# Kernel optimization log

Measured on AMD Instinct MI355X. Metric: run time of the kernel, lower is better.

The kernel has to match this reference:

```python
import jax, jax.numpy as jnp
import numpy as np

N_LEVELS = 16
N_FEATURES = 2
MIN_RES = 16
MAX_RES = 512
HASH_SIZE = 19
TABLE_SIZE = 2 ** HASH_SIZE
# per-level grid resolutions (geometric progression, matches torch buffer)
RESOLUTIONS = [int(MIN_RES * (MAX_RES / MIN_RES) ** (i / (N_LEVELS - 1))) for i in range(N_LEVELS)]
# 8 cube-corner offsets, [8, 3] (same ordering as torch.meshgrid indexing='ij')
OFFSETS = np.stack(np.meshgrid(np.array([0, 1]), np.array([0, 1]), np.array([0, 1]), indexing='ij')).reshape(3, -1).T.astype(np.int64)
PRIMES = np.array([1, 2654435761, 805459861], dtype=np.int64)


def setup_inputs() -> dict:
    key = jax.random.key(0)
    k1, k2 = jax.random.split(key)
    N = 1 << 20  # ~1M sample points (e.g., 4096 rays x 256 samples)
    x = jax.random.uniform(k1, (N, 3), dtype=jnp.float32, minval=-1.0, maxval=1.0)
    tables = jax.random.uniform(k2, (N_LEVELS, TABLE_SIZE, N_FEATURES), dtype=jnp.float32, minval=-1e-4, maxval=1e-4)
    return {"x": x, "tables": tables}


def reference(x, tables):
    x = jnp.clip(x.astype(jnp.float32), -1.0, 1.0)  # [N, 3]
    offsets = jnp.asarray(OFFSETS)                  # [8, 3] int64
    primes = jnp.asarray(PRIMES)                    # [3] int64
    outs = []
    for i, res in enumerate(RESOLUTIONS):
        coords = x * res                            # [N, 3]
        cf = jnp.floor(coords)
        lc = coords - cf                            # fractional part, [N, 3]
        # 8 corner integer coords, wrapped into [0, res): [N, 8, 3]
        corners = (cf.astype(jnp.int64)[:, None, :] + offsets[None]) % res
        corners_f = corners.astype(jnp.float32) / res
        # spatial hash: quantize to [0, 2^18) grid then prime-multiply hash
        q = ((corners_f + 1.0) * 0.5 * (2.0 ** 18)).astype(jnp.int64)
        hashed = (q * primes).sum(-1) % TABLE_SIZE  # [N, 8]
        feats = tables[i][hashed]                   # gather, [N, 8, F]
        # trilinear weights: prod over dims of (1-lc) if offset==0 else lc
        w = jnp.where(offsets[None] == 0, 1.0 - lc[:, None, :], lc[:, None, :]).prod(-1)  # [N, 8]
        outs.append((w[..., None] * feats).sum(1))  # [N, F]
    return jnp.concatenate(outs, axis=-1)           # [N, L*F]
```

## Files before the change

### kernel.cpp

```cpp
#include <hip/hip_runtime.h>


static constexpr int      kNLevels   = 16;
static constexpr unsigned kTableSize = 1u << 19;
static constexpr unsigned kMask      = kTableSize - 1u;
static constexpr unsigned kP1        = 2654435761u;
static constexpr unsigned kP2        = 805459861u;

static constexpr int kNBins = 32768;

typedef float v4f __attribute__((ext_vector_type(4)));
typedef float v2f __attribute__((ext_vector_type(2)));

constexpr int RES_[kNLevels]  = {16, 20, 25, 32, 40, 50, 64, 80,
                                 101, 127, 161, 203, 256, 322, 406, 512};
constexpr int QOFF_[kNLevels] = {0, 16, 36, 61, 93, 133, 183, 247,
                                 327, 428, 555, 716, 919, 1175, 1497, 1903};
static constexpr int kQTot = 2415;

constexpr unsigned qval_rcp(int c, int res) {
    const float r = 1.0f / (float)res;
    const float v = (float)c * r;
    const float s = ((v + 1.0f) * 0.5f) * 262144.0f;
    return (unsigned)s;
}

struct QTab {
    unsigned v[kQTot];
    constexpr QTab() : v{} {
        int o = 0;
        for (int i = 0; i < kNLevels; ++i) {
            for (int c = 0; c < RES_[i]; ++c) v[o + c] = qval_rcp(c, RES_[i]);
            o += RES_[i];
        }
    }
};
__constant__ QTab QT = QTab();

__device__ __forceinline__ void level_idx_w(
    const int i, const unsigned* __restrict__ sq,
    const float px, const float py, const float pz,
    unsigned* __restrict__ idx, float* __restrict__ w)
{
    const int   res  = RES_[i];
    const float resf = (float)res;
    const unsigned* qt = sq + QOFF_[i];

    const float cxf = px * resf, cyf = py * resf, czf = pz * resf;
    const float fx = floorf(cxf), fy = floorf(cyf), fz = floorf(czf);
    const float lx = cxf - fx, ly = cyf - fy, lz = czf - fz;

    const int ix = (int)fx, iy = (int)fy, iz = (int)fz;
    const int cx0 = ix < 0 ? ix + res : (ix >= res ? ix - res : ix);
    const int cy0 = iy < 0 ? iy + res : (iy >= res ? iy - res : iy);
    const int cz0 = iz < 0 ? iz + res : (iz >= res ? iz - res : iz);
    const int cx1 = (cx0 + 1 == res) ? 0 : cx0 + 1;
    const int cy1 = (cy0 + 1 == res) ? 0 : cy0 + 1;
    const int cz1 = (cz0 + 1 == res) ? 0 : cz0 + 1;

    const unsigned qx0 = qt[cx0], qx1 = qt[cx1];
    const unsigned qy0 = qt[cy0], qy1 = qt[cy1];
    const unsigned qz0 = qt[cz0], qz1 = qt[cz1];

    const unsigned hy0 = qy0 * kP1, hy1 = qy1 * kP1;
    const unsigned hz0 = qz0 * kP2, hz1 = qz1 * kP2;

    const float wx0 = 1.0f - lx, wx1 = lx;
    const float wy0 = 1.0f - ly, wy1 = ly;
    const float wz0 = 1.0f - lz, wz1 = lz;

#pragma unroll
    for (int m = 0; m < 8; ++m) {
        const unsigned h = ((m & 4) ? qx1 : qx0) +
                           ((m & 2) ? hy1 : hy0) +
                           ((m & 1) ? hz1 : hz0);
        idx[m] = h & kMask;
        w[m] = (((m & 4) ? wx1 : wx0) * ((m & 2) ? wy1 : wy0)) *
               ((m & 1) ? wz1 : wz0);
    }
}

__device__ __forceinline__ void encode_point(
    const unsigned* __restrict__ sq, const float* __restrict__ tables,
    float* __restrict__ out, const int n)
{
    float px = out ? 0.0f : 0.0f;
    (void)px;
}

__device__ __forceinline__ unsigned spread5(unsigned x) {
    x &= 0x3ffu;
    x = (x | (x << 16)) & 0x30000FFu;
    x = (x | (x << 8))  & 0x300F00Fu;
    x = (x | (x << 4))  & 0x30C30C3u;
    x = (x | (x << 2))  & 0x9249249u;
    return x;
}

__device__ __forceinline__ unsigned point_bin(const float* __restrict__ x, int n) {
    float px = fminf(fmaxf(x[3 * n + 0], -1.0f), 1.0f);
    float py = fminf(fmaxf(x[3 * n + 1], -1.0f), 1.0f);
    float pz = fminf(fmaxf(x[3 * n + 2], -1.0f), 1.0f);
    int cx = (int)((px + 1.0f) * 16.0f); cx = cx > 31 ? 31 : cx;
    int cy = (int)((py + 1.0f) * 16.0f); cy = cy > 31 ? 31 : cy;
    int cz = (int)((pz + 1.0f) * 16.0f); cz = cz > 31 ? 31 : cz;
    return spread5((unsigned)cx) | (spread5((unsigned)cy) << 1) |
           (spread5((unsigned)cz) << 2);
}

__global__ void zero_kernel(unsigned* __restrict__ p, int n) {
    int i = blockIdx.x * 256 + threadIdx.x;
    if (i < n) p[i] = 0u;
}

__global__ void hist_kernel(const float* __restrict__ x,
                            unsigned* __restrict__ counts, int N) {
    int n = blockIdx.x * 256 + threadIdx.x;
    if (n >= N) return;
    atomicAdd(&counts[point_bin(x, n)], 1u);
}

__global__ __launch_bounds__(1024) void scan_kernel(
    const unsigned* __restrict__ counts, unsigned* __restrict__ cursor) {
    __shared__ unsigned sh[1024];
    const int t = threadIdx.x;
    unsigned loc[32];
    unsigned s = 0;
#pragma unroll
    for (int j = 0; j < 32; ++j) { loc[j] = s; s += counts[t * 32 + j]; }
    sh[t] = s;
    __syncthreads();
    for (int off = 1; off < 1024; off <<= 1) {
        unsigned v = (t >= off) ? sh[t - off] : 0u;
        __syncthreads();
        sh[t] += v;
        __syncthreads();
    }
    const unsigned base = sh[t] - s;
#pragma unroll
    for (int j = 0; j < 32; ++j) cursor[t * 32 + j] = base + loc[j];
}

__global__ void scatter_kernel(const float* __restrict__ x,
                               unsigned* __restrict__ cursor,
                               unsigned* __restrict__ perm, int N) {
    int n = blockIdx.x * 256 + threadIdx.x;
    if (n >= N) return;
    unsigned pos = atomicAdd(&cursor[point_bin(x, n)], 1u);
    perm[pos] = (unsigned)n;
}

template <bool SORTED>
__global__ __launch_bounds__(256, 6) void hashenc_kernel_t(
    const float* __restrict__ x,
    const float* __restrict__ tables,
    float* __restrict__ out,
    const unsigned* __restrict__ perm,
    int N)
{
    __shared__ unsigned sq[kQTot];
    for (int t = threadIdx.x; t < kQTot; t += 256) sq[t] = QT.v[t];
    __syncthreads();

    int bid = blockIdx.x;
    if (SORTED) {
        const int nblk = gridDim.x;
        if ((nblk & 7) == 0) bid = (bid & 7) * (nblk >> 3) + (bid >> 3);
    }
    const int g = bid * 256 + threadIdx.x;
    if (g >= N) return;
    const int n = SORTED ? (int)perm[g] : g;

    float px = x[3 * n + 0];
    float py = x[3 * n + 1];
    float pz = x[3 * n + 2];
    px = fminf(fmaxf(px, -1.0f), 1.0f);
    py = fminf(fmaxf(py, -1.0f), 1.0f);
    pz = fminf(fmaxf(pz, -1.0f), 1.0f);

    v4f* op = (v4f*)(out + (size_t)n * (2 * kNLevels));

#pragma unroll
    for (int ip = 0; ip < kNLevels / 2; ++ip) {
        const int iA = 2 * ip, iB = 2 * ip + 1;

        unsigned ia[8], ib[8];
        float    wa[8], wb[8];
        level_idx_w(iA, sq, px, py, pz, ia, wa);
        level_idx_w(iB, sq, px, py, pz, ib, wb);

        const v2f* tA = (const v2f*)tables + (size_t)iA * kTableSize;
        const v2f* tB = (const v2f*)tables + (size_t)iB * kTableSize;

        v2f fa[8], fb[8];
#pragma unroll
        for (int m = 0; m < 8; ++m) fa[m] = tA[ia[m]];
#pragma unroll
        for (int m = 0; m < 8; ++m) fb[m] = tB[ib[m]];

        float a0 = 0.0f, a1 = 0.0f, b0 = 0.0f, b1 = 0.0f;
#pragma unroll
        for (int m = 0; m < 8; ++m) {
            a0 += wa[m] * fa[m].x;
            a1 += wa[m] * fa[m].y;
        }
#pragma unroll
        for (int m = 0; m < 8; ++m) {
            b0 += wb[m] * fb[m].x;
            b1 += wb[m] * fb[m].y;
        }

        v4f v = {a0, a1, b0, b1};
        op[ip] = v;
    }
}

extern "C" void kernel_launch(void* const* d_in, const int* in_sizes, int n_in,
                              void* d_out, int out_size, void* d_ws, size_t ws_size,
                              hipStream_t stream) {
    const float* x      = (const float*)d_in[0];
    const float* tables = (const float*)d_in[1];
    float*       out    = (float*)d_out;
    const int N = in_sizes[0] / 3;
    const int pb = (N + 255) / 256;

    const size_t need = ((size_t)2 * kNBins + (size_t)N) * sizeof(unsigned);
    if (d_ws != nullptr && ws_size >= need) {
        unsigned* counts = (unsigned*)d_ws;
        unsigned* cursor = counts + kNBins;
        unsigned* perm   = cursor + kNBins;

        hipLaunchKernelGGL(zero_kernel, dim3((kNBins + 255) / 256), dim3(256),
                           0, stream, counts, kNBins);
        hipLaunchKernelGGL(hist_kernel, dim3(pb), dim3(256), 0, stream,
                           x, counts, N);
        hipLaunchKernelGGL(scan_kernel, dim3(1), dim3(1024), 0, stream,
                           counts, cursor);
        hipLaunchKernelGGL(scatter_kernel, dim3(pb), dim3(256), 0, stream,
                           x, cursor, perm, N);
        hipLaunchKernelGGL((hashenc_kernel_t<true>), dim3(pb), dim3(256),
                           0, stream, x, tables, out, perm, N);
    } else {
        hipLaunchKernelGGL((hashenc_kernel_t<false>), dim3(pb), dim3(256),
                           0, stream, x, tables, out, nullptr, N);
    }
}
```

Measured before the change: 991.1 us.

## Split hash encoding into per-level-pair blocks over sorted points

The encoding kernel now launches eight times as many blocks. Each block handles one pair of levels (a small level paired with a large one, g and 15-g) for 256 spatially sorted points. Adjacent blocks work on the same level pair, so each block's gathers stay inside two tables, which should improve cache locality and balance the load. The cost is that every point's coordinates and permutation entry are read eight times, outputs are written as scattered 8-byte stores instead of full rows, and resolution is now a runtime value, so constant folding is lost.

```diff
diff --git a/kernel.cpp b/kernel.cpp
--- a/kernel.cpp
+++ b/kernel.cpp
@@ -37,14 +37,17 @@
 };
 __constant__ QTab QT = QTab();
 
-__device__ __forceinline__ void level_idx_w(
-    const int i, const unsigned* __restrict__ sq,
+__constant__ int cRES[kNLevels]  = {16, 20, 25, 32, 40, 50, 64, 80,
+                                    101, 127, 161, 203, 256, 322, 406, 512};
+__constant__ int cQOFF[kNLevels] = {0, 16, 36, 61, 93, 133, 183, 247,
+                                    327, 428, 555, 716, 919, 1175, 1497, 1903};
+
+__device__ __forceinline__ void level_idx_w_rt(
+    const int res, const unsigned* __restrict__ qt,
     const float px, const float py, const float pz,
     unsigned* __restrict__ idx, float* __restrict__ w)
 {
-    const int   res  = RES_[i];
     const float resf = (float)res;
-    const unsigned* qt = sq + QOFF_[i];
 
     const float cxf = px * resf, cyf = py * resf, czf = pz * resf;
     const float fx = floorf(cxf), fy = floorf(cyf), fz = floorf(czf);
@@ -78,14 +81,6 @@
         w[m] = (((m & 4) ? wx1 : wx0) * ((m & 2) ? wy1 : wy0)) *
                ((m & 1) ? wz1 : wz0);
     }
-}
-
-__device__ __forceinline__ void encode_point(
-    const unsigned* __restrict__ sq, const float* __restrict__ tables,
-    float* __restrict__ out, const int n)
-{
-    float px = out ? 0.0f : 0.0f;
-    (void)px;
 }
 
 __device__ __forceinline__ unsigned spread5(unsigned x) {
@@ -150,26 +145,28 @@
     perm[pos] = (unsigned)n;
 }
 
-template <bool SORTED>
-__global__ __launch_bounds__(256, 6) void hashenc_kernel_t(
+__global__ __launch_bounds__(256, 8) void hashenc_pair_kernel(
     const float* __restrict__ x,
     const float* __restrict__ tables,
     float* __restrict__ out,
     const unsigned* __restrict__ perm,
     int N)
 {
-    __shared__ unsigned sq[kQTot];
-    for (int t = threadIdx.x; t < kQTot; t += 256) sq[t] = QT.v[t];
+    const int g    = blockIdx.x & 7;
+    const int pbid = blockIdx.x >> 3;
+    const int iA = g, iB = 15 - g;
+    const int resA = cRES[iA], resB = cRES[iB];
+    const int qoA  = cQOFF[iA], qoB = cQOFF[iB];
+
+    __shared__ unsigned sq[528];
+    const int tot = resA + resB;
+    for (int t = threadIdx.x; t < tot; t += 256)
+        sq[t] = (t < resA) ? QT.v[qoA + t] : QT.v[qoB + (t - resA)];
     __syncthreads();
 
-    int bid = blockIdx.x;
-    if (SORTED) {
-        const int nblk = gridDim.x;
-        if ((nblk & 7) == 0) bid = (bid & 7) * (nblk >> 3) + (bid >> 3);
-    }
-    const int g = bid * 256 + threadIdx.x;
-    if (g >= N) return;
-    const int n = SORTED ? (int)perm[g] : g;
+    const int gp = pbid * 256 + threadIdx.x;
+    if (gp >= N) return;
+    const int n = (int)perm[gp];
 
     float px = x[3 * n + 0];
     float py = x[3 * n + 1];
@@ -178,6 +175,57 @@
     py = fminf(fmaxf(py, -1.0f), 1.0f);
     pz = fminf(fmaxf(pz, -1.0f), 1.0f);
 
+    unsigned ia[8], ib[8];
+    float    wa[8], wb[8];
+    level_idx_w_rt(resA, sq,        px, py, pz, ia, wa);
+    level_idx_w_rt(resB, sq + resA, px, py, pz, ib, wb);
+
+    const v2f* tA = (const v2f*)tables + (size_t)iA * kTableSize;
+    const v2f* tB = (const v2f*)tables + (size_t)iB * kTableSize;
+
+    v2f fa[8], fb[8];
+#pragma unroll
+    for (int m = 0; m < 8; ++m) fa[m] = tA[ia[m]];
+#pragma unroll
+    for (int m = 0; m < 8; ++m) fb[m] = tB[ib[m]];
+
+    float a0 = 0.0f, a1 = 0.0f, b0 = 0.0f, b1 = 0.0f;
+#pragma unroll
+    for (int m = 0; m < 8; ++m) {
+        a0 += wa[m] * fa[m].x;
+        a1 += wa[m] * fa[m].y;
+    }
+#pragma unroll
+    for (int m = 0; m < 8; ++m) {
+        b0 += wb[m] * fb[m].x;
+        b1 += wb[m] * fb[m].y;
+    }
+
+    v2f* orow = (v2f*)(out + (size_t)n * (2 * kNLevels));
+    v2f va = {a0, a1}; orow[iA] = va;
+    v2f vb = {b0, b1}; orow[iB] = vb;
+}
+
+__global__ __launch_bounds__(256, 6) void hashenc_full_kernel(
+    const float* __restrict__ x,
+    const float* __restrict__ tables,
+    float* __restrict__ out,
+    int N)
+{
+    __shared__ unsigned sq[kQTot];
+    for (int t = threadIdx.x; t < kQTot; t += 256) sq[t] = QT.v[t];
+    __syncthreads();
+
+    const int n = blockIdx.x * 256 + threadIdx.x;
+    if (n >= N) return;
+
+    float px = x[3 * n + 0];
+    float py = x[3 * n + 1];
+    float pz = x[3 * n + 2];
+    px = fminf(fmaxf(px, -1.0f), 1.0f);
+    py = fminf(fmaxf(py, -1.0f), 1.0f);
+    pz = fminf(fmaxf(pz, -1.0f), 1.0f);
+
     v4f* op = (v4f*)(out + (size_t)n * (2 * kNLevels));
 
 #pragma unroll
@@ -186,8 +234,8 @@
 
         unsigned ia[8], ib[8];
         float    wa[8], wb[8];
-        level_idx_w(iA, sq, px, py, pz, ia, wa);
-        level_idx_w(iB, sq, px, py, pz, ib, wb);
+        level_idx_w_rt(RES_[iA], sq + QOFF_[iA], px, py, pz, ia, wa);
+        level_idx_w_rt(RES_[iB], sq + QOFF_[iB], px, py, pz, ib, wb);
 
         const v2f* tA = (const v2f*)tables + (size_t)iA * kTableSize;
         const v2f* tB = (const v2f*)tables + (size_t)iB * kTableSize;
@@ -238,10 +286,10 @@
                            counts, cursor);
         hipLaunchKernelGGL(scatter_kernel, dim3(pb), dim3(256), 0, stream,
                            x, cursor, perm, N);
-        hipLaunchKernelGGL((hashenc_kernel_t<true>), dim3(pb), dim3(256),
+        hipLaunchKernelGGL(hashenc_pair_kernel, dim3(pb * 8), dim3(256),
                            0, stream, x, tables, out, perm, N);
     } else {
-        hipLaunchKernelGGL((hashenc_kernel_t<false>), dim3(pb), dim3(256),
-                           0, stream, x, tables, out, nullptr, N);
-    }
-}
+        hipLaunchKernelGGL(hashenc_full_kernel, dim3(pb), dim3(256),
+                           0, stream, x, tables, out, N);
+    }
+}
```

New measurement: 1.138 ms. 1.15x slower.

## Scatter sorted points with index and batch four levels of gathers

Applied to the files above, without the earlier changes.

The scatter pass now writes each point's coordinates together with its original index as a float4 into the workspace. The encode kernel can then read the sorted point with one coalesced load instead of an indirect perm lookup followed by a scattered x read. The sorted encode kernel also processes four levels at a time, issuing 32 gathers before any accumulation, with a scheduling barrier to cluster the loads. Launch bounds drop to 4 waves per SIMD to make room for the extra registers. The costs are a larger workspace, a wider scatter write, and lower occupancy.

```diff
diff --git a/kernel.cpp b/kernel.cpp
--- a/kernel.cpp
+++ b/kernel.cpp
@@ -37,14 +37,12 @@
 };
 __constant__ QTab QT = QTab();
 
-__device__ __forceinline__ void level_idx_w(
-    const int i, const unsigned* __restrict__ sq,
+__device__ __forceinline__ void level_idx_w_rt(
+    const int res, const unsigned* __restrict__ qt,
     const float px, const float py, const float pz,
     unsigned* __restrict__ idx, float* __restrict__ w)
 {
-    const int   res  = RES_[i];
     const float resf = (float)res;
-    const unsigned* qt = sq + QOFF_[i];
 
     const float cxf = px * resf, cyf = py * resf, czf = pz * resf;
     const float fx = floorf(cxf), fy = floorf(cyf), fz = floorf(czf);
@@ -78,14 +76,6 @@
         w[m] = (((m & 4) ? wx1 : wx0) * ((m & 2) ? wy1 : wy0)) *
                ((m & 1) ? wz1 : wz0);
     }
-}
-
-__device__ __forceinline__ void encode_point(
-    const unsigned* __restrict__ sq, const float* __restrict__ tables,
-    float* __restrict__ out, const int n)
-{
-    float px = out ? 0.0f : 0.0f;
-    (void)px;
 }
 
 __device__ __forceinline__ unsigned spread5(unsigned x) {
@@ -143,19 +133,18 @@
 
 __global__ void scatter_kernel(const float* __restrict__ x,
                                unsigned* __restrict__ cursor,
-                               unsigned* __restrict__ perm, int N) {
+                               v4f* __restrict__ xs, int N) {
     int n = blockIdx.x * 256 + threadIdx.x;
     if (n >= N) return;
     unsigned pos = atomicAdd(&cursor[point_bin(x, n)], 1u);
-    perm[pos] = (unsigned)n;
-}
-
-template <bool SORTED>
-__global__ __launch_bounds__(256, 6) void hashenc_kernel_t(
-    const float* __restrict__ x,
+    v4f v = {x[3 * n + 0], x[3 * n + 1], x[3 * n + 2], __int_as_float(n)};
+    xs[pos] = v;
+}
+
+__global__ __launch_bounds__(256, 4) void hashenc_sorted_kernel(
+    const v4f* __restrict__ xs,
     const float* __restrict__ tables,
     float* __restrict__ out,
-    const unsigned* __restrict__ perm,
     int N)
 {
     __shared__ unsigned sq[kQTot];
@@ -163,13 +152,72 @@
     __syncthreads();
 
     int bid = blockIdx.x;
-    if (SORTED) {
-        const int nblk = gridDim.x;
-        if ((nblk & 7) == 0) bid = (bid & 7) * (nblk >> 3) + (bid >> 3);
-    }
+    const int nblk = gridDim.x;
+    if ((nblk & 7) == 0) bid = (bid & 7) * (nblk >> 3) + (bid >> 3);
+
     const int g = bid * 256 + threadIdx.x;
     if (g >= N) return;
-    const int n = SORTED ? (int)perm[g] : g;
+
+    const v4f p = xs[g];
+    const int n = __float_as_int(p.w);
+
+    float px = fminf(fmaxf(p.x, -1.0f), 1.0f);
+    float py = fminf(fmaxf(p.y, -1.0f), 1.0f);
+    float pz = fminf(fmaxf(p.z, -1.0f), 1.0f);
+
+    v4f* op = (v4f*)(out + (size_t)n * (2 * kNLevels));
+
+#pragma unroll
+    for (int q = 0; q < 4; ++q) {
+        unsigned id[4][8];
+        float    w[4][8];
+#pragma unroll
+        for (int j = 0; j < 4; ++j) {
+            const int lv = 4 * q + j;
+            level_idx_w_rt(RES_[lv], sq + QOFF_[lv], px, py, pz, id[j], w[j]);
+        }
+
+        v2f f[4][8];
+#pragma unroll
+        for (int j = 0; j < 4; ++j) {
+            const v2f* tb = (const v2f*)tables + (size_t)(4 * q + j) * kTableSize;
+#pragma unroll
+            for (int m = 0; m < 8; ++m) f[j][m] = tb[id[j][m]];
+        }
+        __builtin_amdgcn_sched_group_barrier(0x20 , 32, 0);
+
+#pragma unroll
+        for (int half = 0; half < 2; ++half) {
+            v4f v;
+#pragma unroll
+            for (int j2 = 0; j2 < 2; ++j2) {
+                const int j = 2 * half + j2;
+                float a0 = 0.0f, a1 = 0.0f;
+#pragma unroll
+                for (int m = 0; m < 8; ++m) {
+                    a0 += w[j][m] * f[j][m].x;
+                    a1 += w[j][m] * f[j][m].y;
+                }
+                v[2 * j2 + 0] = a0;
+                v[2 * j2 + 1] = a1;
+            }
+            op[2 * q + half] = v;
+        }
+    }
+}
+
+__global__ __launch_bounds__(256, 6) void hashenc_full_kernel(
+    const float* __restrict__ x,
+    const float* __restrict__ tables,
+    float* __restrict__ out,
+    int N)
+{
+    __shared__ unsigned sq[kQTot];
+    for (int t = threadIdx.x; t < kQTot; t += 256) sq[t] = QT.v[t];
+    __syncthreads();
+
+    const int n = blockIdx.x * 256 + threadIdx.x;
+    if (n >= N) return;
 
     float px = x[3 * n + 0];
     float py = x[3 * n + 1];
@@ -186,8 +234,8 @@
 
         unsigned ia[8], ib[8];
         float    wa[8], wb[8];
-        level_idx_w(iA, sq, px, py, pz, ia, wa);
-        level_idx_w(iB, sq, px, py, pz, ib, wb);
+        level_idx_w_rt(RES_[iA], sq + QOFF_[iA], px, py, pz, ia, wa);
+        level_idx_w_rt(RES_[iB], sq + QOFF_[iB], px, py, pz, ib, wb);
 
         const v2f* tA = (const v2f*)tables + (size_t)iA * kTableSize;
         const v2f* tB = (const v2f*)tables + (size_t)iB * kTableSize;
@@ -224,11 +272,12 @@
     const int N = in_sizes[0] / 3;
     const int pb = (N + 255) / 256;
 
-    const size_t need = ((size_t)2 * kNBins + (size_t)N) * sizeof(unsigned);
+    const size_t need = (size_t)2 * kNBins * sizeof(unsigned)
+                      + (size_t)N * sizeof(v4f);
     if (d_ws != nullptr && ws_size >= need) {
         unsigned* counts = (unsigned*)d_ws;
         unsigned* cursor = counts + kNBins;
-        unsigned* perm   = cursor + kNBins;
+        v4f*      xs     = (v4f*)(cursor + kNBins);
 
         hipLaunchKernelGGL(zero_kernel, dim3((kNBins + 255) / 256), dim3(256),
                            0, stream, counts, kNBins);
@@ -237,11 +286,11 @@
         hipLaunchKernelGGL(scan_kernel, dim3(1), dim3(1024), 0, stream,
                            counts, cursor);
         hipLaunchKernelGGL(scatter_kernel, dim3(pb), dim3(256), 0, stream,
-                           x, cursor, perm, N);
-        hipLaunchKernelGGL((hashenc_kernel_t<true>), dim3(pb), dim3(256),
-                           0, stream, x, tables, out, perm, N);
+                           x, cursor, xs, N);
+        hipLaunchKernelGGL(hashenc_sorted_kernel, dim3(pb), dim3(256),
+                           0, stream, xs, tables, out, N);
     } else {
-        hipLaunchKernelGGL((hashenc_kernel_t<false>), dim3(pb), dim3(256),
-                           0, stream, x, tables, out, nullptr, N);
-    }
-}
+        hipLaunchKernelGGL(hashenc_full_kernel, dim3(pb), dim3(256),
+                           0, stream, x, tables, out, N);
+    }
+}
```

Result: faster. 957.5 us (-3.4%).
